# Performance work log

Measured on AMD Instinct MI355X. Metric: run time of the kernel, lower is better.

## Reference

```python
import jax, jax.numpy as jnp
import numpy as np

NUM_HEADS = 12


def _rel_lookup(rel_pos, size):
    # q_size == k_size == size, table length == 2*size-1: pure gather, no interp
    idx = jnp.arange(size)[:, None] - jnp.arange(size)[None, :] + (size - 1)
    return rel_pos[idx]  # (size, size, head_dim)


def setup_inputs() -> dict:
    key = jax.random.key(0)
    ks = jax.random.split(key, 7)
    B, H, W, C = 8, 32, 32, 768
    return {
        "x": jax.random.normal(ks[0], (B, H, W, C), dtype=jnp.float32),
        "w_qkv": jax.random.normal(ks[1], (C, 3 * C), dtype=jnp.float32) * 0.02,
        "b_qkv": jax.random.normal(ks[2], (3 * C,), dtype=jnp.float32) * 0.02,
        "w_proj": jax.random.normal(ks[3], (C, C), dtype=jnp.float32) * 0.02,
        "b_proj": jax.random.normal(ks[4], (C,), dtype=jnp.float32) * 0.02,
        "rel_pos_h": jax.random.normal(ks[5], (2 * H - 1, C // NUM_HEADS), dtype=jnp.float32) * 0.02,
        "rel_pos_w": jax.random.normal(ks[6], (2 * W - 1, C // NUM_HEADS), dtype=jnp.float32) * 0.02,
    }


def reference(x, w_qkv, b_qkv, w_proj, b_proj, rel_pos_h, rel_pos_w):
    B, H, W, C = x.shape
    nh = NUM_HEADS
    hd = C // nh
    scale = hd ** -0.5

    qkv = x @ w_qkv + b_qkv  # (B,H,W,3C)
    qkv = qkv.reshape(B, H * W, 3, nh, hd).transpose(2, 0, 3, 1, 4)
    qkv = qkv.reshape(3, B * nh, H * W, hd)
    q, k, v = qkv[0], qkv[1], qkv[2]  # each (B*nh, HW, hd)

    attn = jnp.einsum('bqd,bkd->bqk', q * scale, k)  # (B*nh, HW, HW)

    Rh = _rel_lookup(rel_pos_h, H)  # (H,H,hd)
    Rw = _rel_lookup(rel_pos_w, W)  # (W,W,hd)
    r_q = q.reshape(B * nh, H, W, hd)
    rel_h = jnp.einsum('bhwc,hkc->bhwk', r_q, Rh)  # (B*nh,H,W,H)
    rel_w = jnp.einsum('bhwc,wkc->bhwk', r_q, Rw)  # (B*nh,H,W,W)
    attn = (attn.reshape(B * nh, H, W, H, W)
            + rel_h[:, :, :, :, None]
            + rel_w[:, :, :, None, :]).reshape(B * nh, H * W, H * W)

    attn = jax.nn.softmax(attn, axis=-1)
    out = jnp.einsum('bqk,bkd->bqd', attn, v)  # (B*nh, HW, hd)
    out = out.reshape(B, nh, H, W, hd).transpose(0, 2, 3, 1, 4).reshape(B, H, W, C)
    return out @ w_proj + b_proj
```

## Files before the change

kernel.cpp:

```cpp
#include <hip/hip_runtime.h>

typedef unsigned short u16;
typedef unsigned int u32;
typedef __attribute__((ext_vector_type(8))) short short8;
typedef __attribute__((ext_vector_type(4))) float f32x4;
typedef __attribute__((ext_vector_type(4))) u32 u32x4;

__device__ __forceinline__ u16 f2bf(float f) {
  u32 u = __float_as_uint(f);
  return (u16)((u + 0x7FFFu + ((u >> 16) & 1u)) >> 16);
}
__device__ __forceinline__ float bf2f(u16 u) { return __uint_as_float(((u32)u) << 16); }
__device__ __forceinline__ f32x4 zero4() { f32x4 z = {0.f, 0.f, 0.f, 0.f}; return z; }

__device__ __forceinline__ u32 cvt_pk_bf16(float lo, float hi) {
  u32 r;
  asm("v_cvt_pk_bf16_f32 %0, %1, %2" : "=v"(r) : "v"(lo), "v"(hi));
  return r;
}

__device__ __forceinline__ void g2lds16(const void* g, void* l) {
  __builtin_amdgcn_global_load_lds((const __attribute__((address_space(1))) void*)g,
                                   (__attribute__((address_space(3))) void*)l, 16, 0, 0);
}

#define LOG2E 1.44269504088896340736f

__global__ __launch_bounds__(256) void cvt_x_kernel(const float* __restrict__ in,
                                                    u16* __restrict__ out, int n4) {
  int i = blockIdx.x * 256 + threadIdx.x;
  if (i >= n4) return;
  float4 v = ((const float4*)in)[i];
  ushort4 o;
  o.x = f2bf(v.x); o.y = f2bf(v.y); o.z = f2bf(v.z); o.w = f2bf(v.w);
  ((ushort4*)out)[i] = o;
}

__global__ __launch_bounds__(256) void transp_cvt_kernel(const float* __restrict__ in,
                                                         u16* __restrict__ out, int K, int N) {
  __shared__ float t[32][33];
  int n0 = blockIdx.x * 32, k0 = blockIdx.y * 32;
  int tx = threadIdx.x & 31, ty = threadIdx.x >> 5;
#pragma unroll
  for (int r = 0; r < 4; ++r)
    t[ty + r * 8][tx] = in[(size_t)(k0 + ty + r * 8) * N + n0 + tx];
  __syncthreads();
#pragma unroll
  for (int r = 0; r < 4; ++r)
    out[(size_t)(n0 + ty + r * 8) * K + k0 + tx] = f2bf(t[tx][ty + r * 8]);
}

__global__ __launch_bounds__(512, 2) void gemm256_kernel(
    const u16* __restrict__ A, const u16* __restrict__ Bt, const float* __restrict__ bias,
    int M, int N, int K,
    u16* __restrict__ q_out, u16* __restrict__ k_out, u16* __restrict__ vT_out) {
  __shared__ __align__(16) u16 As[2 * 256 * 64];
  __shared__ __align__(16) u16 Bs[2 * 256 * 64];
  const int tid = threadIdx.x;
  const int wid = tid >> 6, lane = tid & 63;
  const int wm = wid >> 2, wn = wid & 3;

  const int nwg = gridDim.x * gridDim.y;
  const int flat = blockIdx.y * gridDim.x + blockIdx.x;
  const int wg = (flat & 7) * (nwg >> 3) + (flat >> 3);
  const int bx = wg % gridDim.x, by = wg / gridDim.x;
  const int m0 = by * 256, n0 = bx * 256;

  const int g = lane >> 4, lc = lane & 15;
  const int lr = g << 2;
  const int sChunk = ((tid & 7) ^ ((tid >> 3) & 7)) * 8;

  f32x4 acc[8][4];
#pragma unroll
  for (int i = 0; i < 8; ++i)
#pragma unroll
    for (int j = 0; j < 4; ++j) acc[i][j] = zero4();

#define STAGE_A(buf, half, ktS)                                                          \
  do {                                                                                   \
    _Pragma("unroll") for (int l = 0; l < 2; ++l)                                        \
        g2lds16(A + (size_t)(m0 + (half) * 128 + l * 64 + (tid >> 3)) * K + (ktS) +      \
                    sChunk,                                                              \
                (char*)As + (buf) * 32768 + (half) * 16384 + l * 8192 + tid * 16);       \
  } while (0)
#define STAGE_B(buf, half, ktS)                                                          \
  do {                                                                                   \
    _Pragma("unroll") for (int l = 0; l < 2; ++l)                                        \
        g2lds16(Bt + (size_t)(n0 + (half) * 128 + l * 64 + (tid >> 3)) * K + (ktS) +     \
                    sChunk,                                                              \
                (char*)Bs + (buf) * 32768 + (half) * 16384 + l * 8192 + tid * 16);       \
  } while (0)

#define PHASE(B_, MQ, NQ)                                                                \
  do {                                                                                   \
    short8 af[4][2], bfr[2][2];                                                          \
    _Pragma("unroll") for (int rr = 0; rr < 4; ++rr) {                                   \
      int row = wm * 128 + (MQ) * 64 + rr * 16 + lc;                                     \
      const char* base = (const char*)As + (B_) * 32768 + row * 128;                     \
      af[rr][0] = *(const short8*)(base + (((0 + g) ^ (lc & 7)) << 4));                  \
      af[rr][1] = *(const short8*)(base + (((4 + g) ^ (lc & 7)) << 4));                  \
    }                                                                                    \
    _Pragma("unroll") for (int jj = 0; jj < 2; ++jj) {                                   \
      int row = wn * 64 + (NQ) * 32 + jj * 16 + lc;                                      \
      const char* base = (const char*)Bs + (B_) * 32768 + row * 128;                     \
      bfr[jj][0] = *(const short8*)(base + (((0 + g) ^ (lc & 7)) << 4));                 \
      bfr[jj][1] = *(const short8*)(base + (((4 + g) ^ (lc & 7)) << 4));                 \
    }                                                                                    \
    __builtin_amdgcn_sched_barrier(0);                                                   \
    __builtin_amdgcn_s_barrier();                                                        \
    asm volatile("s_waitcnt lgkmcnt(0)" ::: "memory");                                   \
    __builtin_amdgcn_sched_barrier(0);                                                   \
    __builtin_amdgcn_s_setprio(1);                                                       \
    _Pragma("unroll") for (int ks = 0; ks < 2; ++ks)                                     \
        _Pragma("unroll") for (int rr = 0; rr < 4; ++rr)                                 \
            _Pragma("unroll") for (int jj = 0; jj < 2; ++jj) acc[(MQ)*4 + rr][(NQ)*2 +   \
                                                                jj] =                    \
                __builtin_amdgcn_mfma_f32_16x16x32_bf16(af[rr][ks], bfr[jj][ks],         \
                                                        acc[(MQ)*4 + rr][(NQ)*2 + jj],  \
                                                        0, 0, 0);                        \
    __builtin_amdgcn_s_setprio(0);                                                       \
    __builtin_amdgcn_sched_barrier(0);                                                   \
    __builtin_amdgcn_s_barrier();                                                        \
    __builtin_amdgcn_sched_barrier(0);                                                   \
  } while (0)

  const int nk = K >> 6;
  STAGE_A(0, 0, 0);
  STAGE_A(0, 1, 0);
  STAGE_B(0, 0, 0);
  STAGE_B(0, 1, 0);
  STAGE_A(1, 0, 64);
  STAGE_A(1, 1, 64);
  STAGE_B(1, 0, 64);
  STAGE_B(1, 1, 64);
  asm volatile("s_waitcnt vmcnt(8)" ::: "memory");
  __builtin_amdgcn_sched_barrier(0);
  __builtin_amdgcn_s_barrier();

  for (int it = 0; it < nk; ++it) {
    const int b = it & 1;
    PHASE(b, 0, 0);
    PHASE(b, 0, 1);
    PHASE(b, 1, 0);
    PHASE(b, 1, 1);
    if (it + 2 < nk) {
      const int kt2 = (it + 2) << 6;
      STAGE_A(b, 0, kt2);
      STAGE_A(b, 1, kt2);
      STAGE_B(b, 0, kt2);
      STAGE_B(b, 1, kt2);
      asm volatile("s_waitcnt vmcnt(8)" ::: "memory");
    } else if (it + 1 < nk) {
      asm volatile("s_waitcnt vmcnt(0)" ::: "memory");
    }
    __builtin_amdgcn_sched_barrier(0);
    __builtin_amdgcn_s_barrier();
  }
#undef PHASE
#undef STAGE_A
#undef STAGE_B

#pragma unroll
  for (int j = 0; j < 4; ++j) {
    int n = n0 + wn * 64 + j * 16 + lc;
    float bv = bias[n];
    int three = n / 768;
    int rem = n - three * 768;
    int head = rem >> 6, d = rem & 63;
#pragma unroll
    for (int i = 0; i < 8; ++i) {
      int mbase = m0 + wm * 128 + i * 16 + lr;
      if (three == 2) {
        int t0 = mbase & 1023;
        int bb = mbase >> 10;
        size_t bh = (size_t)bb * 12 + head;
        ushort4 ov;
        ov.x = f2bf(acc[i][j][0] + bv);
        ov.y = f2bf(acc[i][j][1] + bv);
        ov.z = f2bf(acc[i][j][2] + bv);
        ov.w = f2bf(acc[i][j][3] + bv);
        *(ushort4*)(vT_out + (bh * 64 + d) * 1024 + t0) = ov;
      } else {
#pragma unroll
        for (int r = 0; r < 4; ++r) {
          int m = mbase + r;
          int bb = m >> 10, t = m & 1023;
          size_t bh = (size_t)bb * 12 + head;
          float val = acc[i][j][r] + bv;
          if (three == 0)
            q_out[(bh * 1024 + t) * 64 + d] = f2bf(val * (0.125f * LOG2E));
          else
            k_out[(bh * 1024 + t) * 64 + d] = f2bf(val);
        }
      }
    }
  }
}

__global__ __launch_bounds__(256, 3) void gemm_proj_kernel(
    const u16* __restrict__ A, const u16* __restrict__ Bt, const float* __restrict__ bias,
    int M, int N, int K, float* __restrict__ f_out) {
  __shared__ __align__(16) u16 As[2 * 128 * 32];
  __shared__ __align__(16) u16 Bs[2 * 128 * 32];
  const int tid = threadIdx.x;
  const int w = tid >> 6, lane = tid & 63;

  const int nwg = gridDim.x * gridDim.y;
  const int flat = blockIdx.y * gridDim.x + blockIdx.x;
  const int wg = (flat & 7) * (nwg >> 3) + (flat >> 3);
  const int bx = wg % gridDim.x, by = wg / gridDim.x;
  const int m0 = by * 128, n0 = bx * 128;
  const int wm0 = (w >> 1) * 64, wn0 = (w & 1) * 64;

  f32x4 acc[4][4];
#pragma unroll
  for (int i = 0; i < 4; ++i)
#pragma unroll
    for (int j = 0; j < 4; ++j) acc[i][j] = zero4();

  const int sRow = lane >> 2;
  const int sChunk = ((lane & 3) ^ ((lane >> 3) & 3)) * 8;
  const int cw = ((lane >> 4) << 4) ^ (((lane >> 1) & 3) << 4);
  const int g = lane >> 4, lc = lane & 15;
  const int lr = g << 2;

#define GSTAGE(buf, ktS)                                                                   \
  do {                                                                                     \
    _Pragma("unroll") for (int jj = 0; jj < 4; ++jj) {                                     \
      int i = w + jj * 4;                                                                  \
      if (i < 8)                                                                           \
        g2lds16(A + (size_t)(m0 + i * 16 + sRow) * K + (ktS) + sChunk,                     \
                (char*)As + (buf) * 8192 + i * 1024);                                      \
      else                                                                                 \
        g2lds16(Bt + (size_t)(n0 + (i - 8) * 16 + sRow) * K + (ktS) + sChunk,              \
                (char*)Bs + (buf) * 8192 + (i - 8) * 1024);                                \
    }                                                                                      \
  } while (0)

  const int nk = K >> 5;
  GSTAGE(0, 0);
  GSTAGE(1, 32);
  asm volatile("s_waitcnt vmcnt(4)" ::: "memory");
  __builtin_amdgcn_sched_barrier(0);
  __builtin_amdgcn_s_barrier();

  for (int kti = 0; kti < nk; ++kti) {
    const int cur = kti & 1;
    short8 af[4], bfr[4];
#pragma unroll
    for (int r = 0; r < 4; ++r) {
      af[r] = *(const short8*)((const char*)As + cur * 8192 + (wm0 + r * 16 + lc) * 64 + cw);
      bfr[r] = *(const short8*)((const char*)Bs + cur * 8192 + (wn0 + r * 16 + lc) * 64 + cw);
    }
    __builtin_amdgcn_s_setprio(1);
#pragma unroll
    for (int i = 0; i < 4; ++i)
#pragma unroll
      for (int j = 0; j < 4; ++j)
        acc[i][j] = __builtin_amdgcn_mfma_f32_16x16x32_bf16(af[i], bfr[j], acc[i][j], 0, 0, 0);
    __builtin_amdgcn_s_setprio(0);

    asm volatile("s_waitcnt lgkmcnt(0)" ::: "memory");
    __builtin_amdgcn_sched_barrier(0);
    __builtin_amdgcn_s_barrier();

    if (kti + 2 < nk) {
      GSTAGE(cur, (kti + 2) << 5);
      asm volatile("s_waitcnt vmcnt(4)" ::: "memory");
    } else {
      asm volatile("s_waitcnt vmcnt(0)" ::: "memory");
    }
    __builtin_amdgcn_sched_barrier(0);
    __builtin_amdgcn_s_barrier();
  }
#undef GSTAGE

#pragma unroll
  for (int j = 0; j < 4; ++j) {
    int n = n0 + wn0 + j * 16 + lc;
    float bv = bias[n];
#pragma unroll
    for (int i = 0; i < 4; ++i)
#pragma unroll
      for (int r = 0; r < 4; ++r) {
        int m = m0 + wm0 + i * 16 + lr + r;
        f_out[(size_t)m * N + n] = acc[i][j][r] + bv;
      }
  }
}

__global__ __launch_bounds__(256) void rel_kernel(const u16* __restrict__ qs,
                                                  const float* __restrict__ rph,
                                                  const float* __restrict__ rpw,
                                                  float* __restrict__ relh,
                                                  float* __restrict__ relw) {
  __shared__ __align__(16) float Ts[63 * 68];
  __shared__ __align__(16) u16 Qs[32 * 72];
  const int tid = threadIdx.x;
  const int h = blockIdx.x, bh = blockIdx.y;
  const int mode = blockIdx.z;
  const float* table = mode ? rpw : rph;
  float* out = mode ? relw : relh;
  for (int i = tid; i < (63 * 64) / 4; i += 256) {
    float4 v = ((const float4*)table)[i];
    int row = i >> 4, col = (i & 15) * 4;
    *(float4*)(Ts + row * 68 + col) = v;
  }
  const u16* qrow = qs + ((size_t)bh * 1024 + h * 32) * 64;
  for (int i = tid; i < (32 * 64) / 8; i += 256) {
    uint4 v = ((const uint4*)qrow)[i];
    int row = i >> 3, col = (i & 7) * 8;
    *(uint4*)(Qs + row * 72 + col) = v;
  }
  __syncthreads();
  const int w = tid >> 3;
  const int kx = tid & 7;
  const int base = mode ? w : h;
  float acc0 = 0.f, acc1 = 0.f, acc2 = 0.f, acc3 = 0.f;
  const u16* qp = Qs + w * 72;
#pragma unroll
  for (int dc = 0; dc < 8; ++dc) {
    uint4 qv = *(const uint4*)(qp + dc * 8);
    float qf[8];
    qf[0] = bf2f((u16)(qv.x & 0xffff)); qf[1] = bf2f((u16)(qv.x >> 16));
    qf[2] = bf2f((u16)(qv.y & 0xffff)); qf[3] = bf2f((u16)(qv.y >> 16));
    qf[4] = bf2f((u16)(qv.z & 0xffff)); qf[5] = bf2f((u16)(qv.z >> 16));
    qf[6] = bf2f((u16)(qv.w & 0xffff)); qf[7] = bf2f((u16)(qv.w >> 16));
#pragma unroll
    for (int jj = 0; jj < 4; ++jj) {
      int row = base - (kx + 8 * jj) + 31;
      const float* tp = Ts + row * 68 + dc * 8;
      float4 p0 = ((const float4*)tp)[0];
      float4 p1 = ((const float4*)tp)[1];
      float s = qf[0] * p0.x + qf[1] * p0.y + qf[2] * p0.z + qf[3] * p0.w +
                qf[4] * p1.x + qf[5] * p1.y + qf[6] * p1.z + qf[7] * p1.w;
      if (jj == 0) acc0 += s;
      else if (jj == 1) acc1 += s;
      else if (jj == 2) acc2 += s;
      else acc3 += s;
    }
  }
  float* op = out + ((size_t)bh * 1024 + h * 32 + w) * 32 + kx;
  op[0] = acc0 * 8.f;
  op[8] = acc1 * 8.f;
  op[16] = acc2 * 8.f;
  op[24] = acc3 * 8.f;
}

__global__ __launch_bounds__(256) void flash_kernel(
    const u16* __restrict__ qs, const u16* __restrict__ kb, const u16* __restrict__ vT,
    const float* __restrict__ relh, const float* __restrict__ relw, u16* __restrict__ ao) {
  __shared__ __align__(16) u16 Ks[2 * 64 * 64];
  __shared__ __align__(16) u16 Vs[2 * 64 * 64];
  __shared__ __align__(16) float RhS[64 * 33];
  __shared__ __align__(16) u32 PpT[4][32 * 20];
  const int tid = threadIdx.x, wv = tid >> 6, lane = tid & 63;
  const int nwg = gridDim.x * gridDim.y;
  const int flat = blockIdx.y * gridDim.x + blockIdx.x;
  const int wg = (flat & 7) * (nwg >> 3) + (flat >> 3);
  const int qt = wg & 15, bh = wg >> 4;
  const int q0 = qt * 64;
  const int g = lane >> 4, lc = lane & 15;

  const float* rh_g = relh + ((size_t)bh * 1024 + q0) * 32;
  for (int i = tid; i < 64 * 32; i += 256) RhS[(i >> 5) * 33 + (i & 31)] = rh_g[i];

  const size_t qbase = ((size_t)bh * 1024 + q0 + wv * 16 + lc) * 64;
  short8 aq0 = *(const short8*)(qs + qbase + g * 8);
  short8 aq1 = *(const short8*)(qs + qbase + 32 + g * 8);

  const float* rwp = relw + ((size_t)bh * 1024 + q0 + wv * 16 + lc) * 32 + 4 * g;
  float4 rw0 = *(const float4*)(rwp);
  float4 rw1 = *(const float4*)(rwp + 16);
  float rwr[8] = {rw0.x, rw0.y, rw0.z, rw0.w, rw1.x, rw1.y, rw1.z, rw1.w};

  f32x4 o[4];
#pragma unroll
  for (int ct = 0; ct < 4; ++ct) o[ct] = zero4();
  float lsum = 0.f;
  const int rhbase = (wv * 16 + lc) * 33;

  const int stgRow = lane >> 3;
  const int stgChunk = ((lane & 7) ^ (lane >> 3)) * 8;
  u32* pt = &PpT[wv][0];

#define STAGE(buf, ktS)                                                                   \
  do {                                                                                    \
    const int k0s = (ktS) * 64;                                                           \
    _Pragma("unroll") for (int jj = 0; jj < 4; ++jj) {                                    \
      int i = wv + jj * 4;                                                                \
      if (i < 8)                                                                          \
        g2lds16(kb + ((size_t)bh * 1024 + k0s + i * 8 + stgRow) * 64 + stgChunk,          \
                (char*)Ks + (buf) * 8192 + i * 1024);                                     \
      else                                                                                \
        g2lds16(vT + ((size_t)bh * 64 + (i - 8) * 8 + stgRow) * 1024 + k0s + stgChunk,    \
                (char*)Vs + (buf) * 8192 + (i - 8) * 1024);                               \
    }                                                                                     \
  } while (0)

  STAGE(0, 0);
  __syncthreads();

  for (int kt = 0; kt < 16; ++kt) {
    const int cur = kt & 1;
    if (kt < 15) STAGE(cur ^ 1, kt + 1);

    f32x4 s[4];
    __builtin_amdgcn_s_setprio(1);
#pragma unroll
    for (int ct = 0; ct < 4; ++ct) {
      int key = ct * 16 + lc;
      int sw = (key & 7) << 4;
      const char* kp = (const char*)Ks + cur * 8192 + key * 128;
      short8 kf0 = *(const short8*)(kp + ((g * 16) ^ sw));
      short8 kf1 = *(const short8*)(kp + ((64 + g * 16) ^ sw));
      f32x4 z = zero4();
      z = __builtin_amdgcn_mfma_f32_16x16x32_bf16(kf0, aq0, z, 0, 0, 0);
      z = __builtin_amdgcn_mfma_f32_16x16x32_bf16(kf1, aq1, z, 0, 0, 0);
      s[ct] = z;
    }
    __builtin_amdgcn_s_setprio(0);

    float rh0 = RhS[rhbase + kt * 2 + 0];
    float rh1 = RhS[rhbase + kt * 2 + 1];
    float pr[4][4];
#pragma unroll
    for (int ct = 0; ct < 4; ++ct)
#pragma unroll
      for (int r = 0; r < 4; ++r)
        pr[ct][r] = __builtin_amdgcn_exp2f(s[ct][r] + (ct < 2 ? rh0 : rh1) +
                                           rwr[(ct & 1) * 4 + r]);

    lsum += ((pr[0][0] + pr[0][1]) + (pr[0][2] + pr[0][3])) +
            ((pr[1][0] + pr[1][1]) + (pr[1][2] + pr[1][3])) +
            ((pr[2][0] + pr[2][1]) + (pr[2][2] + pr[2][3])) +
            ((pr[3][0] + pr[3][1]) + (pr[3][2] + pr[3][3]));

#pragma unroll
    for (int ct = 0; ct < 4; ++ct) {
      u32 w0 = cvt_pk_bf16(pr[ct][0], pr[ct][1]);
      u32 w1 = cvt_pk_bf16(pr[ct][2], pr[ct][3]);
      pt[(8 * ct + 2 * g + 0) * 20 + lc] = w0;
      pt[(8 * ct + 2 * g + 1) * 20 + lc] = w1;
    }

    union { u32x4 u; short8 s; } pb0, pb1;
#pragma unroll
    for (int p = 0; p < 4; ++p) {
      pb0.u[p] = pt[(4 * g + p) * 20 + lc];
      pb1.u[p] = pt[(16 + 4 * g + p) * 20 + lc];
    }

    __builtin_amdgcn_s_setprio(1);
#pragma unroll
    for (int ct = 0; ct < 4; ++ct) {
      int d = ct * 16 + lc;
      int sw = (d & 7) << 4;
      const char* vp = (const char*)Vs + cur * 8192 + d * 128;
      short8 vf0 = *(const short8*)(vp + ((g * 16) ^ sw));
      short8 vf1 = *(const short8*)(vp + ((64 + g * 16) ^ sw));
      o[ct] = __builtin_amdgcn_mfma_f32_16x16x32_bf16(vf0, pb0.s, o[ct], 0, 0, 0);
      o[ct] = __builtin_amdgcn_mfma_f32_16x16x32_bf16(vf1, pb1.s, o[ct], 0, 0, 0);
    }
    __builtin_amdgcn_s_setprio(0);

    __syncthreads();
  }

  lsum += __shfl_xor(lsum, 16);
  lsum += __shfl_xor(lsum, 32);
  float inv = 1.0f / lsum;

  const int b_ = bh / 12, head = bh - b_ * 12;
  u16* op = ao + ((size_t)b_ * 1024 + q0 + wv * 16 + lc) * 768 + head * 64 + 4 * g;
#pragma unroll
  for (int ct = 0; ct < 4; ++ct) {
    ushort4 ov;
    ov.x = f2bf(o[ct][0] * inv);
    ov.y = f2bf(o[ct][1] * inv);
    ov.z = f2bf(o[ct][2] * inv);
    ov.w = f2bf(o[ct][3] * inv);
    *(ushort4*)(op + ct * 16) = ov;
  }
#undef STAGE
}

extern "C" void kernel_launch(void* const* d_in, const int* in_sizes, int n_in,
                              void* d_out, int out_size, void* d_ws, size_t ws_size,
                              hipStream_t stream) {
  const float* x = (const float*)d_in[0];
  const float* w_qkv = (const float*)d_in[1];
  const float* b_qkv = (const float*)d_in[2];
  const float* w_proj = (const float*)d_in[3];
  const float* b_proj = (const float*)d_in[4];
  const float* rph = (const float*)d_in[5];
  const float* rpw = (const float*)d_in[6];
  (void)in_sizes; (void)n_in; (void)out_size; (void)ws_size;

  char* ws = (char*)d_ws;
  size_t off = 0;
  auto alloc = [&](size_t bytes) {
    void* p = ws + off;
    off += (bytes + 255) & ~(size_t)255;
    return p;
  };
  u16* xb = (u16*)alloc((size_t)8192 * 768 * 2);
  float* relh = (float*)xb;
  u16* wqkvT = (u16*)alloc((size_t)2304 * 768 * 2);
  u16* wprojT = (u16*)alloc((size_t)768 * 768 * 2);
  u16* qsb = (u16*)alloc((size_t)96 * 1024 * 64 * 2);
  u16* kbb = (u16*)alloc((size_t)96 * 1024 * 64 * 2);
  u16* vTb = (u16*)alloc((size_t)96 * 64 * 1024 * 2);
  float* relw = (float*)alloc((size_t)96 * 1024 * 32 * 4);
  u16* ao = (u16*)alloc((size_t)8192 * 768 * 2);

  cvt_x_kernel<<<dim3(8192 * 768 / 4 / 256), 256, 0, stream>>>(x, xb, 8192 * 768 / 4);
  transp_cvt_kernel<<<dim3(2304 / 32, 768 / 32), 256, 0, stream>>>(w_qkv, wqkvT, 768, 2304);
  transp_cvt_kernel<<<dim3(768 / 32, 768 / 32), 256, 0, stream>>>(w_proj, wprojT, 768, 768);
  gemm256_kernel<<<dim3(2304 / 256, 8192 / 256), 512, 0, stream>>>(
      xb, wqkvT, b_qkv, 8192, 2304, 768, qsb, kbb, vTb);
  rel_kernel<<<dim3(32, 96, 2), 256, 0, stream>>>(qsb, rph, rpw, relh, relw);
  flash_kernel<<<dim3(16, 96), 256, 0, stream>>>(qsb, kbb, vTb, relh, relw, ao);
  gemm_proj_kernel<<<dim3(768 / 128, 8192 / 128), 256, 0, stream>>>(
      ao, wprojT, b_proj, 8192, 768, 768, (float*)d_out);
}
```

Before: 183.1 us.

## Shrink QKV GEMM tile to 256x128 with 4x2 wave layout

Changes the QKV projection GEMM tile from 256x256 to 256x128 and rearranges the 8 waves as 4x2 so each wave owns a 64x64 output block. This doubles the grid from 288 to 576 workgroups, which should fill the CUs better (288 is barely above the CU count of a large GPU). It also halves the accumulator registers and shrinks the B LDS buffer. In exchange, per-tile data reuse drops and total global and LDS traffic per output rises. The phase structure becomes two k-substeps per 64-wide k tile.

```diff
diff --git a/kernel.cpp b/kernel.cpp
--- a/kernel.cpp
+++ b/kernel.cpp
@@ -55,69 +55,62 @@
     int M, int N, int K,
     u16* __restrict__ q_out, u16* __restrict__ k_out, u16* __restrict__ vT_out) {
   __shared__ __align__(16) u16 As[2 * 256 * 64];
-  __shared__ __align__(16) u16 Bs[2 * 256 * 64];
+  __shared__ __align__(16) u16 Bs[2 * 128 * 64];
   const int tid = threadIdx.x;
   const int wid = tid >> 6, lane = tid & 63;
-  const int wm = wid >> 2, wn = wid & 3;
+  const int wm = wid >> 1, wn = wid & 1;
 
   const int nwg = gridDim.x * gridDim.y;
   const int flat = blockIdx.y * gridDim.x + blockIdx.x;
   const int wg = (flat & 7) * (nwg >> 3) + (flat >> 3);
   const int bx = wg % gridDim.x, by = wg / gridDim.x;
-  const int m0 = by * 256, n0 = bx * 256;
+  const int m0 = by * 256, n0 = bx * 128;
 
   const int g = lane >> 4, lc = lane & 15;
   const int lr = g << 2;
   const int sChunk = ((tid & 7) ^ ((tid >> 3) & 7)) * 8;
 
-  f32x4 acc[8][4];
-#pragma unroll
-  for (int i = 0; i < 8; ++i)
+  f32x4 acc[4][4];
+#pragma unroll
+  for (int i = 0; i < 4; ++i)
 #pragma unroll
     for (int j = 0; j < 4; ++j) acc[i][j] = zero4();
 
-#define STAGE_A(buf, half, ktS)                                                          \
+#define STAGE_A(buf, ktS)                                                                \
+  do {                                                                                   \
+    _Pragma("unroll") for (int l = 0; l < 4; ++l)                                        \
+        g2lds16(A + (size_t)(m0 + l * 64 + (tid >> 3)) * K + (ktS) + sChunk,             \
+                (char*)As + (buf) * 32768 + l * 8192 + tid * 16);                        \
+  } while (0)
+#define STAGE_B(buf, ktS)                                                                \
   do {                                                                                   \
     _Pragma("unroll") for (int l = 0; l < 2; ++l)                                        \
-        g2lds16(A + (size_t)(m0 + (half) * 128 + l * 64 + (tid >> 3)) * K + (ktS) +      \
-                    sChunk,                                                              \
-                (char*)As + (buf) * 32768 + (half) * 16384 + l * 8192 + tid * 16);       \
+        g2lds16(Bt + (size_t)(n0 + l * 64 + (tid >> 3)) * K + (ktS) + sChunk,            \
+                (char*)Bs + (buf) * 16384 + l * 8192 + tid * 16);                        \
   } while (0)
-#define STAGE_B(buf, half, ktS)                                                          \
+
+#define PHASE(B_, ks)                                                                    \
   do {                                                                                   \
-    _Pragma("unroll") for (int l = 0; l < 2; ++l)                                        \
-        g2lds16(Bt + (size_t)(n0 + (half) * 128 + l * 64 + (tid >> 3)) * K + (ktS) +     \
-                    sChunk,                                                              \
-                (char*)Bs + (buf) * 32768 + (half) * 16384 + l * 8192 + tid * 16);       \
-  } while (0)
-
-#define PHASE(B_, MQ, NQ)                                                                \
-  do {                                                                                   \
-    short8 af[4][2], bfr[2][2];                                                          \
+    short8 af[4], bfr[4];                                                                \
     _Pragma("unroll") for (int rr = 0; rr < 4; ++rr) {                                   \
-      int row = wm * 128 + (MQ) * 64 + rr * 16 + lc;                                     \
-      const char* base = (const char*)As + (B_) * 32768 + row * 128;                     \
-      af[rr][0] = *(const short8*)(base + (((0 + g) ^ (lc & 7)) << 4));                  \
-      af[rr][1] = *(const short8*)(base + (((4 + g) ^ (lc & 7)) << 4));                  \
+      int row = wm * 64 + rr * 16 + lc;                                                  \
+      af[rr] = *(const short8*)((const char*)As + (B_) * 32768 + row * 128 +             \
+                                (((((ks) << 2) | g) ^ (lc & 7)) << 4));                  \
     }                                                                                    \
-    _Pragma("unroll") for (int jj = 0; jj < 2; ++jj) {                                   \
-      int row = wn * 64 + (NQ) * 32 + jj * 16 + lc;                                      \
-      const char* base = (const char*)Bs + (B_) * 32768 + row * 128;                     \
-      bfr[jj][0] = *(const short8*)(base + (((0 + g) ^ (lc & 7)) << 4));                 \
-      bfr[jj][1] = *(const short8*)(base + (((4 + g) ^ (lc & 7)) << 4));                 \
+    _Pragma("unroll") for (int jj = 0; jj < 4; ++jj) {                                   \
+      int row = wn * 64 + jj * 16 + lc;                                                  \
+      bfr[jj] = *(const short8*)((const char*)Bs + (B_) * 16384 + row * 128 +            \
+                                 (((((ks) << 2) | g) ^ (lc & 7)) << 4));                 \
     }                                                                                    \
     __builtin_amdgcn_sched_barrier(0);                                                   \
     __builtin_amdgcn_s_barrier();                                                        \
     asm volatile("s_waitcnt lgkmcnt(0)" ::: "memory");                                   \
     __builtin_amdgcn_sched_barrier(0);                                                   \
     __builtin_amdgcn_s_setprio(1);                                                       \
-    _Pragma("unroll") for (int ks = 0; ks < 2; ++ks)                                     \
-        _Pragma("unroll") for (int rr = 0; rr < 4; ++rr)                                 \
-            _Pragma("unroll") for (int jj = 0; jj < 2; ++jj) acc[(MQ)*4 + rr][(NQ)*2 +   \
-                                                                jj] =                    \
-                __builtin_amdgcn_mfma_f32_16x16x32_bf16(af[rr][ks], bfr[jj][ks],         \
-                                                        acc[(MQ)*4 + rr][(NQ)*2 + jj],  \
-                                                        0, 0, 0);                        \
+    _Pragma("unroll") for (int rr = 0; rr < 4; ++rr)                                     \
+        _Pragma("unroll") for (int jj = 0; jj < 4; ++jj) acc[rr][jj] =                   \
+            __builtin_amdgcn_mfma_f32_16x16x32_bf16(af[rr], bfr[jj], acc[rr][jj],        \
+                                                    0, 0, 0);                            \
     __builtin_amdgcn_s_setprio(0);                                                       \
     __builtin_amdgcn_sched_barrier(0);                                                   \
     __builtin_amdgcn_s_barrier();                                                        \
@@ -125,31 +118,23 @@
   } while (0)
 
   const int nk = K >> 6;
-  STAGE_A(0, 0, 0);
-  STAGE_A(0, 1, 0);
-  STAGE_B(0, 0, 0);
-  STAGE_B(0, 1, 0);
-  STAGE_A(1, 0, 64);
-  STAGE_A(1, 1, 64);
-  STAGE_B(1, 0, 64);
-  STAGE_B(1, 1, 64);
-  asm volatile("s_waitcnt vmcnt(8)" ::: "memory");
+  STAGE_A(0, 0);
+  STAGE_B(0, 0);
+  STAGE_A(1, 64);
+  STAGE_B(1, 64);
+  asm volatile("s_waitcnt vmcnt(6)" ::: "memory");
   __builtin_amdgcn_sched_barrier(0);
   __builtin_amdgcn_s_barrier();
 
   for (int it = 0; it < nk; ++it) {
     const int b = it & 1;
-    PHASE(b, 0, 0);
-    PHASE(b, 0, 1);
-    PHASE(b, 1, 0);
-    PHASE(b, 1, 1);
+    PHASE(b, 0);
+    PHASE(b, 1);
     if (it + 2 < nk) {
       const int kt2 = (it + 2) << 6;
-      STAGE_A(b, 0, kt2);
-      STAGE_A(b, 1, kt2);
-      STAGE_B(b, 0, kt2);
-      STAGE_B(b, 1, kt2);
-      asm volatile("s_waitcnt vmcnt(8)" ::: "memory");
+      STAGE_A(b, kt2);
+      STAGE_B(b, kt2);
+      asm volatile("s_waitcnt vmcnt(6)" ::: "memory");
     } else if (it + 1 < nk) {
       asm volatile("s_waitcnt vmcnt(0)" ::: "memory");
     }
@@ -168,8 +153,8 @@
     int rem = n - three * 768;
     int head = rem >> 6, d = rem & 63;
 #pragma unroll
-    for (int i = 0; i < 8; ++i) {
-      int mbase = m0 + wm * 128 + i * 16 + lr;
+    for (int i = 0; i < 4; ++i) {
+      int mbase = m0 + wm * 64 + i * 16 + lr;
       if (three == 2) {
         int t0 = mbase & 1023;
         int bb = mbase >> 10;
@@ -517,7 +502,7 @@
   cvt_x_kernel<<<dim3(8192 * 768 / 4 / 256), 256, 0, stream>>>(x, xb, 8192 * 768 / 4);
   transp_cvt_kernel<<<dim3(2304 / 32, 768 / 32), 256, 0, stream>>>(w_qkv, wqkvT, 768, 2304);
   transp_cvt_kernel<<<dim3(768 / 32, 768 / 32), 256, 0, stream>>>(w_proj, wprojT, 768, 768);
-  gemm256_kernel<<<dim3(2304 / 256, 8192 / 256), 512, 0, stream>>>(
+  gemm256_kernel<<<dim3(2304 / 128, 8192 / 256), 512, 0, stream>>>(
       xb, wqkvT, b_qkv, 8192, 2304, 768, qsb, kbb, vTb);
   rel_kernel<<<dim3(32, 96, 2), 256, 0, stream>>>(qsb, rph, rpw, relh, relw);
   flash_kernel<<<dim3(16, 96), 256, 0, stream>>>(qsb, kbb, vTb, relh, relw, ao);
```

Result: faster. 170.8 us (-6.7%).
